# Kernel optimization log

Hardware: AMD Instinct MI355X
Metric: run time of the kernel (lower is better)

The kernel has to match this reference:

```python
import jax, jax.numpy as jnp
import numpy as np

B, S, DIM = 2, 2048, 2048
QH, KVH = 32, 8
HD = DIM // QH            # 64
KV_DIM = HD * KVH         # 512
MAX_LEN = 2048
SCALE = HD ** -0.5
NEG_INF = -1e30


def _rope_cache(seq_len, head_dim, max_len, theta=10000.0, factor=8.0):
    # faithful to generate_sin_cos_pos_emb (causal branch, offset=0),
    # cache built at max_len then sliced to seq_len by the caller
    idx = np.arange(0, head_dim, 2, dtype=np.float64) / head_dim
    inv_freq = 1.0 / theta ** idx
    if factor > 1.0:
        seq_eff = max(max_len, max_len)  # generate called with seq_len=max_length
        adj = (factor * seq_eff / max_len - (factor - 1.0)) ** (head_dim / (head_dim - 2.0))
        inv_freq = 1.0 / (theta * adj) ** idx
    pos = np.arange(0, max_len, dtype=np.float64)
    freqs = np.einsum('i,j->ij', pos, inv_freq)
    emb = np.concatenate([freqs, freqs], axis=-1)  # [max_len, head_dim]
    cos = jnp.asarray(np.cos(emb)[:seq_len], dtype=jnp.float32)
    sin = jnp.asarray(np.sin(emb)[:seq_len], dtype=jnp.float32)
    return cos, sin


def _rotate_half(x):
    x1, x2 = jnp.split(x, 2, axis=-1)
    return jnp.concatenate([-x2, x1], axis=-1)


def _apply_rope(x, cos, sin):
    # x: [B, H, S, D]; cos/sin: [S, D]
    return x * cos + _rotate_half(x) * sin


def setup_inputs() -> dict:
    key = jax.random.key(0)
    ks = jax.random.split(key, 11)
    s = 0.02
    return {
        'query': jax.random.normal(ks[0], (B, S, DIM), jnp.float32),
        'key':   jax.random.normal(ks[1], (B, S, DIM), jnp.float32),
        'value': jax.random.normal(ks[2], (B, S, DIM), jnp.float32),
        'w_q': jax.random.normal(ks[3], (DIM, DIM), jnp.float32) * s,
        'b_q': jnp.zeros((DIM,), jnp.float32),
        'w_k': jax.random.normal(ks[4], (DIM, KV_DIM), jnp.float32) * s,
        'b_k': jnp.zeros((KV_DIM,), jnp.float32),
        'w_v': jax.random.normal(ks[5], (DIM, KV_DIM), jnp.float32) * s,
        'b_v': jnp.zeros((KV_DIM,), jnp.float32),
        'w_o': jax.random.normal(ks[6], (DIM, DIM), jnp.float32) * s,
        'b_o': jnp.zeros((DIM,), jnp.float32),
    }


def reference(query, key, value, w_q, b_q, w_k, b_k, w_v, b_v, w_o, b_o):
    # projections (weights stored as [in, out])
    q = query @ w_q + b_q                                    # [B,S,DIM]
    k = key   @ w_k + b_k                                    # [B,S,KV_DIM]
    v = value @ w_v + b_v                                    # [B,S,KV_DIM]

    q = q.reshape(B, S, QH, HD).transpose(0, 2, 1, 3)        # [B,QH,S,HD]
    k = k.reshape(B, S, KVH, HD).transpose(0, 2, 1, 3)       # [B,KVH,S,HD]
    v = v.reshape(B, S, KVH, HD).transpose(0, 2, 1, 3)       # [B,KVH,S,HD]

    cos, sin = _rope_cache(S, HD, MAX_LEN)
    q = _apply_rope(q, cos, sin)
    k = _apply_rope(k, cos, sin)

    # GQA: group queries per kv head (equivalent to repeat_interleave on K/V)
    G = QH // KVH
    qg = q.reshape(B, KVH, G, S, HD)
    scores = jnp.einsum('bhgqd,bhkd->bhgqk', qg, k) * SCALE  # [B,KVH,G,S,S]
    causal = jnp.tril(jnp.ones((S, S), dtype=bool))
    scores = jnp.where(causal, scores, NEG_INF)
    probs = jax.nn.softmax(scores, axis=-1)
    ctx = jnp.einsum('bhgqk,bhkd->bhgqd', probs, v)          # [B,KVH,G,S,HD]
    ctx = ctx.reshape(B, QH, S, HD).transpose(0, 2, 1, 3).reshape(B, S, DIM)
    return ctx @ w_o + b_o                                   # [B,S,DIM]
```

## Files before the change

kernel.cpp:

```cpp
#include <hip/hip_runtime.h>
#include <hip/hip_bf16.h>

typedef __hip_bfloat16 bf16_t;
typedef __attribute__((ext_vector_type(8))) short bf16x8;
typedef __attribute__((ext_vector_type(4))) float f32x4;

#define S_LEN   2048
#define D_MODEL 2048
#define N_QH    32
#define N_KVH   8
#define HEAD_D  64
#define KV_D    512
#define M_ROWS  4096
#define QK_SCALE (0.125f * 1.44269504088896340736f)
#define NQT     16

struct __align__(8) bf16x4s { bf16_t x, y, z, w; };

__global__ void prep_kernel(const float* __restrict__ wq, const float* __restrict__ wk,
                            const float* __restrict__ wv, const float* __restrict__ wo,
                            bf16_t* __restrict__ tq, bf16_t* __restrict__ tk,
                            bf16_t* __restrict__ tv, bf16_t* __restrict__ to,
                            const float* __restrict__ query, const float* __restrict__ key_,
                            const float* __restrict__ value,
                            bf16_t* __restrict__ qbf, bf16_t* __restrict__ kbf,
                            bf16_t* __restrict__ vbf,
                            float* __restrict__ cosT, float* __restrict__ sinT) {
    const int bx = blockIdx.x, t = threadIdx.x;
    if (bx < 10240) {
        __shared__ float tile[32][33];
        const float* W; bf16_t* Wt; int N, nb, kt;
        if (bx < 4096)      { W = wq; Wt = tq; N = D_MODEL; nb = bx & 63;          kt = bx >> 6; }
        else if (bx < 5120) { int i = bx - 4096; W = wk; Wt = tk; N = KV_D; nb = i & 15; kt = i >> 4; }
        else if (bx < 6144) { int i = bx - 5120; W = wv; Wt = tv; N = KV_D; nb = i & 15; kt = i >> 4; }
        else                { int i = bx - 6144; W = wo; Wt = to; N = D_MODEL; nb = i & 63; kt = i >> 6; }
        const int K = D_MODEL;
        int n0 = nb * 32, k0 = kt * 32;
        int tx = t & 31, ty = t >> 5;
#pragma unroll
        for (int i = 0; i < 4; i++) {
            int r = ty + i * 8;
            tile[r][tx] = W[(size_t)(k0 + r) * N + n0 + tx];
        }
        __syncthreads();
#pragma unroll
        for (int i = 0; i < 4; i++) {
            int r = ty + i * 8;
            Wt[(size_t)(n0 + r) * K + k0 + tx] = __float2bfloat16(tile[tx][r]);
        }
        return;
    }
    if (bx < 10304) {
        int blk = bx - 10240;
        int j = t & 31;
        double invf = pow(10000.0, -(double)(2 * j) / 64.0);
#pragma unroll
        for (int i = 0; i < 4; i++) {
            int pos = blk * 32 + i * 8 + (t >> 5);
            double a = (double)pos * invf;
            cosT[pos * 32 + j] = (float)cos(a);
            sinT[pos * 32 + j] = (float)sin(a);
        }
        return;
    }
    const int per = M_ROWS * D_MODEL / 4;
    int tid = (bx - 10304) * 256 + t;
    for (int i = tid; i < 3 * per; i += 1536 * 256) {
        const float* src; bf16_t* dst; int off;
        if (i < per)          { src = query; dst = qbf; off = i; }
        else if (i < 2 * per) { src = key_;  dst = kbf; off = i - per; }
        else                  { src = value; dst = vbf; off = i - 2 * per; }
        float4 v = ((const float4*)src)[off];
        bf16x4s o;
        o.x = __float2bfloat16(v.x);
        o.y = __float2bfloat16(v.y);
        o.z = __float2bfloat16(v.z);
        o.w = __float2bfloat16(v.w);
        ((bf16x4s*)dst)[off] = o;
    }
}

__device__ __forceinline__ void async_copy16(const bf16_t* g, bf16_t* l) {
    __builtin_amdgcn_global_load_lds((const __attribute__((address_space(1))) void*)g,
                                     (__attribute__((address_space(3))) void*)l, 16, 0, 0);
}

template <int ROPE, int OUTF32, int QSCALE>
__global__ __launch_bounds__(256, 2)
void gqa_gemm_kernel(const bf16_t* __restrict__ A, const bf16_t* __restrict__ Bt,
                     const float* __restrict__ bias, void* __restrict__ Cout,
                     int M, int N, int K,
                     const float* __restrict__ cosT, const float* __restrict__ sinT) {
    __shared__ __align__(16) bf16_t As[128 * 64];
    __shared__ __align__(16) bf16_t Bs[128 * 64];

    const int t = threadIdx.x;
    const int bx = blockIdx.x;
    const int xcd = bx & 7, j = bx >> 3;
    const int am0 = (((xcd >> 1) << 3) + (j >> 3)) * 128;
    const int bn0 = (((xcd & 1) << 3) + (j & 7)) * 128;

    const int l = t & 63, w = t >> 6;
    const int wr = w >> 1, wc = w & 1;
    const int lr = l & 15, lk = l >> 4;

    f32x4 acc[4][4];
#pragma unroll
    for (int i = 0; i < 4; i++)
#pragma unroll
        for (int jx = 0; jx < 4; jx++) acc[i][jx] = (f32x4)0.0f;

    const int r0 = t >> 3;
    const int c  = (t & 7) ^ (r0 & 7);
    const bf16_t* aptr = A + (size_t)(am0 + r0) * K + c * 8;
    const bf16_t* bptr = Bt + (size_t)(bn0 + r0) * K + c * 8;
    bf16_t* aLds = As + r0 * 64 + (t & 7) * 8;
    bf16_t* bLds = Bs + r0 * 64 + (t & 7) * 8;

    for (int k0 = 0; k0 < K; k0 += 64) {
#pragma unroll
        for (int s = 0; s < 4; ++s) {
            async_copy16(aptr + (size_t)(s * 32) * K + k0, aLds + s * 2048);
            async_copy16(bptr + (size_t)(s * 32) * K + k0, bLds + s * 2048);
        }
        __syncthreads();

        bf16x8 af[4][2], bfr[4][2];
#pragma unroll
        for (int mi = 0; mi < 4; mi++)
#pragma unroll
            for (int ks = 0; ks < 2; ks++)
                af[mi][ks] = *(const bf16x8*)&As[(wr * 64 + mi * 16 + lr) * 64 +
                                 ((ks * 32 + lk * 8) ^ ((lr & 7) << 3))];
#pragma unroll
        for (int ni = 0; ni < 4; ni++)
#pragma unroll
            for (int ks = 0; ks < 2; ks++)
                bfr[ni][ks] = *(const bf16x8*)&Bs[(wc * 64 + ni * 16 + lr) * 64 +
                                  ((ks * 32 + lk * 8) ^ ((lr & 7) << 3))];
#pragma unroll
        for (int mi = 0; mi < 4; mi++)
#pragma unroll
            for (int ni = 0; ni < 4; ni++)
#pragma unroll
                for (int ks = 0; ks < 2; ks++)
                    acc[mi][ni] = __builtin_amdgcn_mfma_f32_16x16x32_bf16(
                        af[mi][ks], bfr[ni][ks], acc[mi][ni], 0, 0, 0);
        __syncthreads();
    }

#pragma unroll
    for (int mi = 0; mi < 4; mi++) {
#pragma unroll
        for (int reg = 0; reg < 4; reg++) {
            int row = am0 + wr * 64 + mi * 16 + lk * 4 + reg;
            if (OUTF32) {
                float* out = (float*)Cout;
#pragma unroll
                for (int ni = 0; ni < 4; ni++) {
                    int col = bn0 + wc * 64 + ni * 16 + lr;
                    out[(size_t)row * N + col] = acc[mi][ni][reg] + bias[col];
                }
            } else if (ROPE) {
                bf16_t* out = (bf16_t*)Cout;
                int pos = row & (S_LEN - 1);
#pragma unroll
                for (int np = 0; np < 2; np++) {
                    int jj = np * 16 + lr;
                    float cs = cosT[pos * 32 + jj];
                    float sn = sinT[pos * 32 + jj];
                    int col1 = bn0 + wc * 64 + np * 16 + lr;
                    float x1 = acc[mi][np][reg] + bias[col1];
                    float x2 = acc[mi][np + 2][reg] + bias[col1 + 32];
                    float o1 = x1 * cs - x2 * sn;
                    float o2 = x2 * cs + x1 * sn;
                    if (QSCALE) { o1 *= QK_SCALE; o2 *= QK_SCALE; }
                    out[(size_t)row * N + col1]      = __float2bfloat16(o1);
                    out[(size_t)row * N + col1 + 32] = __float2bfloat16(o2);
                }
            } else {
                bf16_t* out = (bf16_t*)Cout;
#pragma unroll
                for (int ni = 0; ni < 4; ni++) {
                    int col = bn0 + wc * 64 + ni * 16 + lr;
                    out[(size_t)row * N + col] =
                        __float2bfloat16(acc[mi][ni][reg] + bias[col]);
                }
            }
        }
    }
}

__global__ __launch_bounds__(256, 2)
void gqa_qkv_kernel(const bf16_t* __restrict__ Qbf, const bf16_t* __restrict__ Kbf,
                    const bf16_t* __restrict__ Vbf,
                    const bf16_t* __restrict__ Wtq, const bf16_t* __restrict__ Wtk,
                    const bf16_t* __restrict__ Wtv,
                    const float* __restrict__ bq, const float* __restrict__ bk,
                    const float* __restrict__ bv,
                    bf16_t* __restrict__ Qout, bf16_t* __restrict__ Kout,
                    bf16_t* __restrict__ VtOut,
                    const float* __restrict__ cosT, const float* __restrict__ sinT) {
    __shared__ __align__(16) char smem[128 * 140 * 2];
    bf16_t* As = (bf16_t*)smem;
    bf16_t* Bs = (bf16_t*)(smem + 16384);
    bf16_t* TT = (bf16_t*)smem;

    const int t = threadIdx.x, bx = blockIdx.x;
    constexpr int K = D_MODEL;

    int am0, bn0, mode;
    const bf16_t *A, *Bt; const float* bias;
    if (bx < 512) {
        int xcd = bx & 7, j = bx >> 3;
        am0 = (((xcd >> 1) << 3) + (j >> 3)) * 128;
        bn0 = (((xcd & 1) << 3) + (j & 7)) * 128;
        A = Qbf; Bt = Wtq; bias = bq; mode = 0;
    } else {
        int idx = bx - 512;
        int z = idx >> 7;
        int xcd = idx & 7, jj = (idx & 127) >> 3;
        am0 = (xcd * 4 + (jj & 3)) * 128;
        bn0 = (jj >> 2) * 128;
        A = z ? Vbf : Kbf; Bt = z ? Wtv : Wtk; bias = z ? bv : bk; mode = z ? 2 : 1;
    }

    const int l = t & 63, w = t >> 6;
    const int wr = w >> 1, wc = w & 1;
    const int lr = l & 15, lk = l >> 4;

    f32x4 acc[4][4];
#pragma unroll
    for (int i = 0; i < 4; i++)
#pragma unroll
        for (int jx = 0; jx < 4; jx++) acc[i][jx] = (f32x4)0.0f;

    const int r0 = t >> 3;
    const int c  = (t & 7) ^ (r0 & 7);
    const bf16_t* aptr = A + (size_t)(am0 + r0) * K + c * 8;
    const bf16_t* bptr = Bt + (size_t)(bn0 + r0) * K + c * 8;
    bf16_t* aLds = As + r0 * 64 + (t & 7) * 8;
    bf16_t* bLds = Bs + r0 * 64 + (t & 7) * 8;

    for (int k0 = 0; k0 < K; k0 += 64) {
#pragma unroll
        for (int s = 0; s < 4; ++s) {
            async_copy16(aptr + (size_t)(s * 32) * K + k0, aLds + s * 2048);
            async_copy16(bptr + (size_t)(s * 32) * K + k0, bLds + s * 2048);
        }
        __syncthreads();

        bf16x8 af[4][2], bfr[4][2];
#pragma unroll
        for (int mi = 0; mi < 4; mi++)
#pragma unroll
            for (int ks = 0; ks < 2; ks++)
                af[mi][ks] = *(const bf16x8*)&As[(wr * 64 + mi * 16 + lr) * 64 +
                                 ((ks * 32 + lk * 8) ^ ((lr & 7) << 3))];
#pragma unroll
        for (int ni = 0; ni < 4; ni++)
#pragma unroll
            for (int ks = 0; ks < 2; ks++)
                bfr[ni][ks] = *(const bf16x8*)&Bs[(wc * 64 + ni * 16 + lr) * 64 +
                                  ((ks * 32 + lk * 8) ^ ((lr & 7) << 3))];
#pragma unroll
        for (int mi = 0; mi < 4; mi++)
#pragma unroll
            for (int ni = 0; ni < 4; ni++)
#pragma unroll
                for (int ks = 0; ks < 2; ks++)
                    acc[mi][ni] = __builtin_amdgcn_mfma_f32_16x16x32_bf16(
                        af[mi][ks], bfr[ni][ks], acc[mi][ni], 0, 0, 0);
        __syncthreads();
    }

    if (mode == 2) {
#pragma unroll
        for (int mi = 0; mi < 4; mi++)
#pragma unroll
            for (int ni = 0; ni < 4; ni++) {
                int colL = wc * 64 + ni * 16 + lr;
                float bz = bias[bn0 + colL];
                bf16x4s pk;
                pk.x = __float2bfloat16(acc[mi][ni][0] + bz);
                pk.y = __float2bfloat16(acc[mi][ni][1] + bz);
                pk.z = __float2bfloat16(acc[mi][ni][2] + bz);
                pk.w = __float2bfloat16(acc[mi][ni][3] + bz);
                *(bf16x4s*)&TT[colL * 140 + wr * 64 + mi * 16 + lk * 4] = pk;
            }
        __syncthreads();
        const int colL = t >> 1, s0 = (t & 1) * 64;
        const int cg = bn0 + colL;
        const int bI = am0 >> 11;
        bf16_t* dst = VtOut + ((size_t)(bI * N_KVH + (cg >> 6)) * HEAD_D + (cg & 63)) * S_LEN
                      + (am0 & (S_LEN - 1)) + s0;
        const bf16_t* src = &TT[colL * 140 + s0];
#pragma unroll
        for (int i = 0; i < 8; i++)
            *(bf16x8*)(dst + i * 8) = *(const bf16x8*)(src + i * 8);
        return;
    }

    const int N = (mode == 0) ? D_MODEL : KV_D;
    bf16_t* out = (mode == 0) ? Qout : Kout;
    const float qs = (mode == 0) ? QK_SCALE : 1.0f;
#pragma unroll
    for (int mi = 0; mi < 4; mi++)
#pragma unroll
        for (int reg = 0; reg < 4; reg++) {
            int row = am0 + wr * 64 + mi * 16 + lk * 4 + reg;
            int pos = row & (S_LEN - 1);
#pragma unroll
            for (int np = 0; np < 2; np++) {
                int jj = np * 16 + lr;
                float cs = cosT[pos * 32 + jj];
                float sn = sinT[pos * 32 + jj];
                int col1 = bn0 + wc * 64 + np * 16 + lr;
                float x1 = acc[mi][np][reg] + bias[col1];
                float x2 = acc[mi][np + 2][reg] + bias[col1 + 32];
                out[(size_t)row * N + col1]      = __float2bfloat16((x1 * cs - x2 * sn) * qs);
                out[(size_t)row * N + col1 + 32] = __float2bfloat16((x2 * cs + x1 * sn) * qs);
            }
        }
}

__device__ __forceinline__ void stage_K8(const bf16_t* KB, bf16_t* dst, int kt, int t) {
    const int skey = t >> 3;
    const int c    = (t & 7) ^ (skey & 7);
    async_copy16(KB + (size_t)(kt * 64 + skey) * KV_D + c * 8, dst + t * 8);
}
__device__ __forceinline__ void stage_V8(const bf16_t* VTb, bf16_t* dst, int kt, int t) {
    const int sd = t >> 3;
    const int c  = (t & 7) ^ (sd & 7);
    async_copy16(VTb + (size_t)sd * S_LEN + kt * 64 + c * 8, dst + t * 8);
}

__global__ __launch_bounds__(512, 4)
void gqa_attn_kernel(const bf16_t* __restrict__ Q, const bf16_t* __restrict__ Kb,
                     const bf16_t* __restrict__ VT, bf16_t* __restrict__ Ctx) {
    __shared__ __align__(16) bf16_t Ks[2][64 * 64];
    __shared__ __align__(16) bf16_t Vs[2][64 * 64];
    __shared__ __align__(16) bf16_t Pw[8][16 * 72];

    const int t = threadIdx.x, l = t & 63, w = t >> 6;
    const int lr = l & 15, lk = l >> 4;

    const int flat = blockIdx.x;
    const int xcd = flat & 7, j0 = flat >> 3;
    const int qt  = NQT - 1 - (j0 >> 3);
    const int rem = j0 & 7;
    const int combo = xcd * 2 + (rem >> 2);
    const int b   = combo >> 3;
    const int kvh = combo & 7;
    const int h   = kvh * 4 + (rem & 3);

    bf16x8 vones;
#pragma unroll
    for (int i = 0; i < 8; i++) vones[i] = (short)0x3F80;

    const bf16_t* KB  = Kb + (size_t)b * S_LEN * KV_D + kvh * HEAD_D;
    const bf16_t* VTb = VT + ((size_t)(b * N_KVH + kvh) * HEAD_D) * S_LEN;

    const int q0w = qt * 128 + w * 16;
    const int qg  = q0w + lr;

    bf16x8 qf[2];
    {
        const bf16_t* qrow = Q + ((size_t)(b * S_LEN + qg)) * D_MODEL + h * HEAD_D;
        qf[0] = *(const bf16x8*)(qrow + lk * 8);
        qf[1] = *(const bf16x8*)(qrow + 32 + lk * 8);
    }

    f32x4 oaccT[4];
    f32x4 oaccS = (f32x4)0.0f;
#pragma unroll
    for (int df = 0; df < 4; df++) oaccT[df] = (f32x4)0.0f;

    const int nkt = 2 * qt + 2;

    stage_K8(KB, Ks[0], 0, t);
    stage_V8(VTb, Vs[0], 0, t);
    __syncthreads();

    int cur = 0;
    for (int kt = 0; kt < nkt; ++kt) {
        const bool pre = (kt + 1 < nkt);
        if (pre) {
            stage_K8(KB, Ks[cur ^ 1], kt + 1, t);
            stage_V8(VTb, Vs[cur ^ 1], kt + 1, t);
        }

        if (kt * 64 <= q0w + 15) {
            const bool diag = (kt * 64 + 63 > q0w);

            f32x4 sfrT[4];
#pragma unroll
            for (int ni = 0; ni < 4; ni++) sfrT[ni] = (f32x4)0.0f;
            __builtin_amdgcn_s_setprio(1);
#pragma unroll
            for (int ni = 0; ni < 4; ni++)
#pragma unroll
                for (int ks = 0; ks < 2; ks++) {
                    bf16x8 kf = *(const bf16x8*)&Ks[cur][(ni * 16 + lr) * 64 +
                                    ((ks * 32 + lk * 8) ^ ((lr & 7) << 3))];
                    sfrT[ni] = __builtin_amdgcn_mfma_f32_16x16x32_bf16(kf, qf[ks],
                                                                       sfrT[ni], 0, 0, 0);
                }
            __builtin_amdgcn_s_setprio(0);

#pragma unroll
            for (int ni = 0; ni < 4; ni++) {
                float sc0 = sfrT[ni][0], sc1 = sfrT[ni][1];
                float sc2 = sfrT[ni][2], sc3 = sfrT[ni][3];
                if (diag) {
                    int kbase = kt * 64 + ni * 16 + lk * 4;
                    if (kbase + 0 > qg) sc0 = -1e30f;
                    if (kbase + 1 > qg) sc1 = -1e30f;
                    if (kbase + 2 > qg) sc2 = -1e30f;
                    if (kbase + 3 > qg) sc3 = -1e30f;
                }
                float e0 = exp2f(sc0), e1 = exp2f(sc1);
                float e2 = exp2f(sc2), e3 = exp2f(sc3);
                unsigned u0 = __builtin_bit_cast(unsigned, e0);
                unsigned u1 = __builtin_bit_cast(unsigned, e1);
                unsigned u2 = __builtin_bit_cast(unsigned, e2);
                unsigned u3 = __builtin_bit_cast(unsigned, e3);
                uint2 pk;
                pk.x = (u0 >> 16) | (u1 & 0xFFFF0000u);
                pk.y = (u2 >> 16) | (u3 & 0xFFFF0000u);
                *(uint2*)&Pw[w][lr * 72 + ni * 16 + lk * 4] = pk;
            }

            __builtin_amdgcn_s_setprio(1);
#pragma unroll
            for (int ks = 0; ks < 2; ks++) {
                bf16x8 pf = *(const bf16x8*)&Pw[w][lr * 72 + ks * 32 + lk * 8];
                oaccS = __builtin_amdgcn_mfma_f32_16x16x32_bf16(vones, pf, oaccS, 0, 0, 0);
#pragma unroll
                for (int df = 0; df < 4; df++) {
                    bf16x8 vf = *(const bf16x8*)&Vs[cur][(df * 16 + lr) * 64 +
                                    ((ks * 32 + lk * 8) ^ ((lr & 7) << 3))];
                    oaccT[df] = __builtin_amdgcn_mfma_f32_16x16x32_bf16(vf, pf,
                                        oaccT[df], 0, 0, 0);
                }
            }
            __builtin_amdgcn_s_setprio(0);
        }

        __syncthreads();
        cur ^= 1;
    }

    {
        float inv = 1.0f / oaccS[0];
        bf16_t* crow = Ctx + ((size_t)(b * S_LEN + qg)) * D_MODEL + h * HEAD_D;
#pragma unroll
        for (int df = 0; df < 4; df++) {
            bf16x4s ov;
            ov.x = __float2bfloat16(oaccT[df][0] * inv);
            ov.y = __float2bfloat16(oaccT[df][1] * inv);
            ov.z = __float2bfloat16(oaccT[df][2] * inv);
            ov.w = __float2bfloat16(oaccT[df][3] * inv);
            *(bf16x4s*)(crow + df * 16 + lk * 4) = ov;
        }
    }
}

extern "C" void kernel_launch(void* const* d_in, const int* in_sizes, int n_in,
                              void* d_out, int out_size, void* d_ws, size_t ws_size,
                              hipStream_t stream) {
    const float* query = (const float*)d_in[0];
    const float* key_  = (const float*)d_in[1];
    const float* value = (const float*)d_in[2];
    const float* w_q = (const float*)d_in[3];
    const float* b_q = (const float*)d_in[4];
    const float* w_k = (const float*)d_in[5];
    const float* b_k = (const float*)d_in[6];
    const float* w_v = (const float*)d_in[7];
    const float* b_v = (const float*)d_in[8];
    const float* w_o = (const float*)d_in[9];
    const float* b_o = (const float*)d_in[10];
    float* out = (float*)d_out;

    char* ws = (char*)d_ws;
    bf16_t* qbf  = (bf16_t*)(ws);
    bf16_t* qb   = (bf16_t*)(ws + (size_t)(16 << 20));
    bf16_t* kb   = (bf16_t*)(ws + (size_t)(32 << 20));
    bf16_t* vt   = (bf16_t*)(ws + (size_t)(36 << 20));
    bf16_t* wtq  = (bf16_t*)(ws + (size_t)(40 << 20));
    bf16_t* wtk  = (bf16_t*)(ws + (size_t)(48 << 20));
    bf16_t* wtv  = (bf16_t*)(ws + (size_t)(50 << 20));
    bf16_t* wto  = (bf16_t*)(ws + (size_t)(52 << 20));
    float* cosT  = (float*)(ws + (size_t)(60 << 20));
    float* sinT  = (float*)(ws + (size_t)(60 << 20) + (256 << 10));
    bf16_t* kbf  = (bf16_t*)(ws + (size_t)(61 << 20));
    bf16_t* vbf  = (bf16_t*)(ws + (size_t)(77 << 20));

    prep_kernel<<<11840, 256, 0, stream>>>(w_q, w_k, w_v, w_o, wtq, wtk, wtv, wto,
                                           query, key_, value, qbf, kbf, vbf, cosT, sinT);

    gqa_qkv_kernel<<<768, 256, 0, stream>>>(qbf, kbf, vbf, wtq, wtk, wtv,
                                            b_q, b_k, b_v, qb, kb, vt, cosT, sinT);

    gqa_attn_kernel<<<1024, 512, 0, stream>>>(qb, kb, vt, qbf);

    gqa_gemm_kernel<0, 1, 0><<<512, 256, 0, stream>>>(
        qbf, wto, b_o, out, M_ROWS, D_MODEL, D_MODEL, cosT, sinT);
}
```

Baseline: 203.0 us.

## Switch attention kernel to 32x32x16 MFMA with 4 waves of 32 query rows

```diff
diff --git a/kernel.cpp b/kernel.cpp
--- a/kernel.cpp
+++ b/kernel.cpp
@@ -4,6 +4,7 @@
 typedef __hip_bfloat16 bf16_t;
 typedef __attribute__((ext_vector_type(8))) short bf16x8;
 typedef __attribute__((ext_vector_type(4))) float f32x4;
+typedef __attribute__((ext_vector_type(16))) float f32x16;
 
 #define S_LEN   2048
 #define D_MODEL 2048
@@ -324,26 +325,33 @@
         }
 }
 
-__device__ __forceinline__ void stage_K8(const bf16_t* KB, bf16_t* dst, int kt, int t) {
+__device__ __forceinline__ void stage_K4(const bf16_t* KB, bf16_t* dst, int kt, int t) {
     const int skey = t >> 3;
     const int c    = (t & 7) ^ (skey & 7);
-    async_copy16(KB + (size_t)(kt * 64 + skey) * KV_D + c * 8, dst + t * 8);
-}
-__device__ __forceinline__ void stage_V8(const bf16_t* VTb, bf16_t* dst, int kt, int t) {
+#pragma unroll
+    for (int s = 0; s < 2; ++s)
+        async_copy16(KB + (size_t)(kt * 64 + s * 32 + skey) * KV_D + c * 8,
+                     dst + s * 2048 + t * 8);
+}
+__device__ __forceinline__ void stage_V4(const bf16_t* VTb, bf16_t* dst, int kt, int t) {
     const int sd = t >> 3;
     const int c  = (t & 7) ^ (sd & 7);
-    async_copy16(VTb + (size_t)sd * S_LEN + kt * 64 + c * 8, dst + t * 8);
-}
-
-__global__ __launch_bounds__(512, 4)
+#pragma unroll
+    for (int s = 0; s < 2; ++s)
+        async_copy16(VTb + (size_t)(s * 32 + sd) * S_LEN + kt * 64 + c * 8,
+                     dst + s * 2048 + t * 8);
+}
+
+__global__ __launch_bounds__(256, 3)
 void gqa_attn_kernel(const bf16_t* __restrict__ Q, const bf16_t* __restrict__ Kb,
                      const bf16_t* __restrict__ VT, bf16_t* __restrict__ Ctx) {
     __shared__ __align__(16) bf16_t Ks[2][64 * 64];
     __shared__ __align__(16) bf16_t Vs[2][64 * 64];
-    __shared__ __align__(16) bf16_t Pw[8][16 * 72];
+    __shared__ __align__(16) bf16_t Pw[4][32 * 72];
 
     const int t = threadIdx.x, l = t & 63, w = t >> 6;
-    const int lr = l & 15, lk = l >> 4;
+    const int lq = l & 31;
+    const int hi = l >> 5;
 
     const int flat = blockIdx.x;
     const int xcd = flat & 7, j0 = flat >> 3;
@@ -354,93 +362,96 @@
     const int kvh = combo & 7;
     const int h   = kvh * 4 + (rem & 3);
 
-    bf16x8 vones;
-#pragma unroll
-    for (int i = 0; i < 8; i++) vones[i] = (short)0x3F80;
-
     const bf16_t* KB  = Kb + (size_t)b * S_LEN * KV_D + kvh * HEAD_D;
     const bf16_t* VTb = VT + ((size_t)(b * N_KVH + kvh) * HEAD_D) * S_LEN;
 
-    const int q0w = qt * 128 + w * 16;
-    const int qg  = q0w + lr;
-
-    bf16x8 qf[2];
+    const int q0w = qt * 128 + w * 32;
+    const int qg  = q0w + lq;
+
+    bf16x8 qf[4];
     {
         const bf16_t* qrow = Q + ((size_t)(b * S_LEN + qg)) * D_MODEL + h * HEAD_D;
-        qf[0] = *(const bf16x8*)(qrow + lk * 8);
-        qf[1] = *(const bf16x8*)(qrow + 32 + lk * 8);
-    }
-
-    f32x4 oaccT[4];
-    f32x4 oaccS = (f32x4)0.0f;
-#pragma unroll
-    for (int df = 0; df < 4; df++) oaccT[df] = (f32x4)0.0f;
+#pragma unroll
+        for (int s = 0; s < 4; s++)
+            qf[s] = *(const bf16x8*)(qrow + s * 16 + hi * 8);
+    }
+
+    f32x16 oaccT[2];
+    oaccT[0] = (f32x16)0.0f;
+    oaccT[1] = (f32x16)0.0f;
+    float lrow = 0.f;
 
     const int nkt = 2 * qt + 2;
 
-    stage_K8(KB, Ks[0], 0, t);
-    stage_V8(VTb, Vs[0], 0, t);
+    stage_K4(KB, Ks[0], 0, t);
+    stage_V4(VTb, Vs[0], 0, t);
     __syncthreads();
 
     int cur = 0;
     for (int kt = 0; kt < nkt; ++kt) {
         const bool pre = (kt + 1 < nkt);
         if (pre) {
-            stage_K8(KB, Ks[cur ^ 1], kt + 1, t);
-            stage_V8(VTb, Vs[cur ^ 1], kt + 1, t);
-        }
-
-        if (kt * 64 <= q0w + 15) {
+            stage_K4(KB, Ks[cur ^ 1], kt + 1, t);
+            stage_V4(VTb, Vs[cur ^ 1], kt + 1, t);
+        }
+
+        if (kt * 64 <= q0w + 31) {
             const bool diag = (kt * 64 + 63 > q0w);
 
-            f32x4 sfrT[4];
-#pragma unroll
-            for (int ni = 0; ni < 4; ni++) sfrT[ni] = (f32x4)0.0f;
+            f32x16 sfr[2];
+            sfr[0] = (f32x16)0.0f;
+            sfr[1] = (f32x16)0.0f;
             __builtin_amdgcn_s_setprio(1);
 #pragma unroll
-            for (int ni = 0; ni < 4; ni++)
-#pragma unroll
-                for (int ks = 0; ks < 2; ks++) {
-                    bf16x8 kf = *(const bf16x8*)&Ks[cur][(ni * 16 + lr) * 64 +
-                                    ((ks * 32 + lk * 8) ^ ((lr & 7) << 3))];
-                    sfrT[ni] = __builtin_amdgcn_mfma_f32_16x16x32_bf16(kf, qf[ks],
-                                                                       sfrT[ni], 0, 0, 0);
+            for (int kh = 0; kh < 2; kh++)
+#pragma unroll
+                for (int s = 0; s < 4; s++) {
+                    bf16x8 kf = *(const bf16x8*)&Ks[cur][(kh * 32 + lq) * 64 +
+                                    ((s * 16 + hi * 8) ^ ((lq & 7) << 3))];
+                    sfr[kh] = __builtin_amdgcn_mfma_f32_32x32x16_bf16(kf, qf[s],
+                                                                      sfr[kh], 0, 0, 0);
                 }
             __builtin_amdgcn_s_setprio(0);
 
-#pragma unroll
-            for (int ni = 0; ni < 4; ni++) {
-                float sc0 = sfrT[ni][0], sc1 = sfrT[ni][1];
-                float sc2 = sfrT[ni][2], sc3 = sfrT[ni][3];
-                if (diag) {
-                    int kbase = kt * 64 + ni * 16 + lk * 4;
-                    if (kbase + 0 > qg) sc0 = -1e30f;
-                    if (kbase + 1 > qg) sc1 = -1e30f;
-                    if (kbase + 2 > qg) sc2 = -1e30f;
-                    if (kbase + 3 > qg) sc3 = -1e30f;
+            float rs = 0.f;
+#pragma unroll
+            for (int kh = 0; kh < 2; kh++)
+#pragma unroll
+                for (int rq = 0; rq < 4; rq++) {
+                    int keybase = kt * 64 + kh * 32 + rq * 8 + hi * 4;
+                    float sc0 = sfr[kh][rq * 4 + 0];
+                    float sc1 = sfr[kh][rq * 4 + 1];
+                    float sc2 = sfr[kh][rq * 4 + 2];
+                    float sc3 = sfr[kh][rq * 4 + 3];
+                    if (diag) {
+                        if (keybase + 0 > qg) sc0 = -1e30f;
+                        if (keybase + 1 > qg) sc1 = -1e30f;
+                        if (keybase + 2 > qg) sc2 = -1e30f;
+                        if (keybase + 3 > qg) sc3 = -1e30f;
+                    }
+                    float e0 = exp2f(sc0), e1 = exp2f(sc1);
+                    float e2 = exp2f(sc2), e3 = exp2f(sc3);
+                    rs += (e0 + e1) + (e2 + e3);
+                    unsigned u0 = __builtin_bit_cast(unsigned, e0);
+                    unsigned u1 = __builtin_bit_cast(unsigned, e1);
+                    unsigned u2 = __builtin_bit_cast(unsigned, e2);
+                    unsigned u3 = __builtin_bit_cast(unsigned, e3);
+                    uint2 pk;
+                    pk.x = (u0 >> 16) | (u1 & 0xFFFF0000u);
+                    pk.y = (u2 >> 16) | (u3 & 0xFFFF0000u);
+                    *(uint2*)&Pw[w][lq * 72 + kh * 32 + rq * 8 + hi * 4] = pk;
                 }
-                float e0 = exp2f(sc0), e1 = exp2f(sc1);
-                float e2 = exp2f(sc2), e3 = exp2f(sc3);
-                unsigned u0 = __builtin_bit_cast(unsigned, e0);
-                unsigned u1 = __builtin_bit_cast(unsigned, e1);
-                unsigned u2 = __builtin_bit_cast(unsigned, e2);
-                unsigned u3 = __builtin_bit_cast(unsigned, e3);
-                uint2 pk;
-                pk.x = (u0 >> 16) | (u1 & 0xFFFF0000u);
-                pk.y = (u2 >> 16) | (u3 & 0xFFFF0000u);
-                *(uint2*)&Pw[w][lr * 72 + ni * 16 + lk * 4] = pk;
-            }
+            lrow += rs;
 
             __builtin_amdgcn_s_setprio(1);
 #pragma unroll
-            for (int ks = 0; ks < 2; ks++) {
-                bf16x8 pf = *(const bf16x8*)&Pw[w][lr * 72 + ks * 32 + lk * 8];
-                oaccS = __builtin_amdgcn_mfma_f32_16x16x32_bf16(vones, pf, oaccS, 0, 0, 0);
-#pragma unroll
-                for (int df = 0; df < 4; df++) {
-                    bf16x8 vf = *(const bf16x8*)&Vs[cur][(df * 16 + lr) * 64 +
-                                    ((ks * 32 + lk * 8) ^ ((lr & 7) << 3))];
-                    oaccT[df] = __builtin_amdgcn_mfma_f32_16x16x32_bf16(vf, pf,
+            for (int kk = 0; kk < 4; kk++) {
+                bf16x8 pf = *(const bf16x8*)&Pw[w][lq * 72 + kk * 16 + hi * 8];
+#pragma unroll
+                for (int df = 0; df < 2; df++) {
+                    bf16x8 vf = *(const bf16x8*)&Vs[cur][(df * 32 + lq) * 64 +
+                                    ((kk * 16 + hi * 8) ^ ((lq & 7) << 3))];
+                    oaccT[df] = __builtin_amdgcn_mfma_f32_32x32x16_bf16(vf, pf,
                                         oaccT[df], 0, 0, 0);
                 }
             }
@@ -452,17 +463,20 @@
     }
 
     {
-        float inv = 1.0f / oaccS[0];
+        float lsum = lrow + __shfl_xor(lrow, 32);
+        float inv = 1.0f / lsum;
         bf16_t* crow = Ctx + ((size_t)(b * S_LEN + qg)) * D_MODEL + h * HEAD_D;
 #pragma unroll
-        for (int df = 0; df < 4; df++) {
-            bf16x4s ov;
-            ov.x = __float2bfloat16(oaccT[df][0] * inv);
-            ov.y = __float2bfloat16(oaccT[df][1] * inv);
-            ov.z = __float2bfloat16(oaccT[df][2] * inv);
-            ov.w = __float2bfloat16(oaccT[df][3] * inv);
-            *(bf16x4s*)(crow + df * 16 + lk * 4) = ov;
-        }
+        for (int df = 0; df < 2; df++)
+#pragma unroll
+            for (int rq = 0; rq < 4; rq++) {
+                bf16x4s ov;
+                ov.x = __float2bfloat16(oaccT[df][rq * 4 + 0] * inv);
+                ov.y = __float2bfloat16(oaccT[df][rq * 4 + 1] * inv);
+                ov.z = __float2bfloat16(oaccT[df][rq * 4 + 2] * inv);
+                ov.w = __float2bfloat16(oaccT[df][rq * 4 + 3] * inv);
+                *(bf16x4s*)(crow + df * 32 + rq * 8 + hi * 4) = ov;
+            }
     }
 }
 
@@ -502,7 +516,7 @@
     gqa_qkv_kernel<<<768, 256, 0, stream>>>(qbf, kbf, vbf, wtq, wtk, wtv,
                                             b_q, b_k, b_v, qb, kb, vt, cosT, sinT);
 
-    gqa_attn_kernel<<<1024, 512, 0, stream>>>(qb, kb, vt, qbf);
+    gqa_attn_kernel<<<1024, 256, 0, stream>>>(qb, kb, vt, qbf);
 
     gqa_gemm_kernel<0, 1, 0><<<512, 256, 0, stream>>>(
         qbf, wto, b_o, out, M_ROWS, D_MODEL, D_MODEL, cosT, sinT);
```

Result: no change. 202.4 us, median of 2 (-0.3%).
